# Kernel optimization log

Hardware: AMD Instinct MI355X
Metric: run time of the kernel (lower is better)

The kernel has to match this reference:

```python
import jax, jax.numpy as jnp
import numpy as np

N = 1_000_000      # total action rows
S = 250_000        # number of segments (intersections)
D_IN = 64
D_H = 128


def _res_block(x, W, b, P=None):
    # y = relu(x @ W + b); residual add (projected if dims differ)
    y = jax.nn.relu(x @ W + b)
    res = x if P is None else x @ P
    return y + res


def setup_inputs() -> dict:
    key = jax.random.key(0)
    ks = jax.random.split(key, 16)
    sc = 0.02
    x = jax.random.normal(ks[0], (N, D_IN), dtype=jnp.float32)
    index = jnp.sort(jax.random.randint(ks[1], (N,), 0, S)).astype(jnp.int64)
    return {
        "x": x,
        "index": index,
        # value in-stack (1 block, D_IN -> D_H, projected residual)
        "v_in_W": jax.random.normal(ks[2], (D_IN, D_H), jnp.float32) * sc,
        "v_in_b": jnp.zeros((D_H,), jnp.float32),
        "v_in_P": jax.random.normal(ks[3], (D_IN, D_H), jnp.float32) * sc,
        # value out-stack (1 block, D_H -> D_H, identity residual)
        "v_out_W": jax.random.normal(ks[4], (D_H, D_H), jnp.float32) * sc,
        "v_out_b": jnp.zeros((D_H,), jnp.float32),
        # value head linear D_H -> 1
        "v_lin_W": jax.random.normal(ks[5], (D_H, 1), jnp.float32) * sc,
        "v_lin_b": jnp.zeros((1,), jnp.float32),
        # advantage stack (2 blocks: D_IN->D_H projected, D_H->D_H identity)
        "a_W0": jax.random.normal(ks[6], (D_IN, D_H), jnp.float32) * sc,
        "a_b0": jnp.zeros((D_H,), jnp.float32),
        "a_P0": jax.random.normal(ks[7], (D_IN, D_H), jnp.float32) * sc,
        "a_W1": jax.random.normal(ks[8], (D_H, D_H), jnp.float32) * sc,
        "a_b1": jnp.zeros((D_H,), jnp.float32),
        # advantage head linear D_H -> 1
        "a_lin_W": jax.random.normal(ks[9], (D_H, 1), jnp.float32) * sc,
        "a_lin_b": jnp.zeros((1,), jnp.float32),
    }


def reference(x, index, v_in_W, v_in_b, v_in_P, v_out_W, v_out_b, v_lin_W,
              v_lin_b, a_W0, a_b0, a_P0, a_W1, a_b1, a_lin_W, a_lin_b):
    idx = index.astype(jnp.int32)

    # ---- value stream ----
    h = _res_block(x, v_in_W, v_in_b, v_in_P)               # [N, D_H]
    agg = jax.ops.segment_sum(h, idx, num_segments=S)       # [S, D_H]
    h2 = _res_block(agg, v_out_W, v_out_b)                  # [S, D_H]
    sv = h2 @ v_lin_W + v_lin_b                             # [S, 1]
    state_values = sv[idx]                                  # [N, 1] gather-back

    # ---- advantage stream ----
    a = _res_block(x, a_W0, a_b0, a_P0)                     # [N, D_H]
    a = _res_block(a, a_W1, a_b1)                           # [N, D_H]
    adv = a @ a_lin_W + a_lin_b                             # [N, 1]
    ones = jnp.ones((adv.shape[0],), adv.dtype)
    cnt = jax.ops.segment_sum(ones, idx, num_segments=S)    # [S]
    seg_sum = jax.ops.segment_sum(adv, idx, num_segments=S)  # [S, 1]
    seg_mean = seg_sum / jnp.maximum(cnt, 1.0)[:, None]      # [S, 1]
    adv_centered = adv - seg_mean[idx]                       # [N, 1]

    action_values = (state_values + adv_centered).squeeze(-1)  # [N]
    return action_values, index
```

## Files before the change

kernel.cpp:

```cpp
#include <hip/hip_runtime.h>

typedef _Float16 f16;
typedef _Float16 f16x8 __attribute__((ext_vector_type(8)));
typedef _Float16 f16x4v __attribute__((ext_vector_type(4)));
typedef float    f32x4 __attribute__((ext_vector_type(4)));
typedef int      i32x4 __attribute__((ext_vector_type(4)));

#define NROWS 1000000
#define DIN   64
#define DH    128
#define SEGS  250000
#define SPB   64

#define MFMA16(a, b, c) __builtin_amdgcn_mfma_f32_16x16x32_f16((a), (b), (c), 0, 0, 0)

__global__ void k_bounds(const int* __restrict__ idx,
                         int* __restrict__ row_start, int N) {
  int r = blockIdx.x * blockDim.x + threadIdx.x;
  if (r >= N) return;
  int cur  = min(max(idx[r], 0), SEGS - 1);
  int prev = (r == 0) ? -1 : min(max(idx[r - 1], 0), SEGS - 1);
  for (int s = prev + 1; s <= cur; ++s) row_start[s] = r;
  if (r == N - 1) {
    for (int s = cur + 1; s <= SEGS; ++s) row_start[s] = N;
  }
}

__global__ void k_pack(const float* __restrict__ W, f16* __restrict__ out, int K) {
  const int T = K >> 5;
  int i = blockIdx.x * blockDim.x + threadIdx.x;
  if (i >= K * DH) return;
  int e = i & 7, l = (i >> 3) & 63, f = i >> 9;
  int t = f % T, cb = f / T;
  int k = t * 32 + ((l >> 4) << 3) + e;
  int c = cb * 16 + (l & 15);
  out[i] = (f16)W[k * DH + c];
}

__device__ __forceinline__ f16x8 ldfrag(const f16* __restrict__ p, int f, int lane) {
  return *(const f16x8*)(p + (((size_t)f * 64 + lane) << 3));
}

__device__ __forceinline__ f16x8 cvt8(f32x4 u0, f32x4 u1) {
  f16x8 r;
  r[0] = (f16)u0[0]; r[1] = (f16)u0[1]; r[2] = (f16)u0[2]; r[3] = (f16)u0[3];
  r[4] = (f16)u1[0]; r[5] = (f16)u1[1]; r[6] = (f16)u1[2]; r[7] = (f16)u1[3];
  return r;
}

__global__ __launch_bounds__(512) void k_fused(
    const float* __restrict__ x, const int* __restrict__ idx,
    const int* __restrict__ row_start,
    const f16* __restrict__ vWp, const f16* __restrict__ vPp,
    const f16* __restrict__ aW0p, const f16* __restrict__ aP0p,
    const f16* __restrict__ aW1p, const f16* __restrict__ voWp,
    const float* __restrict__ vb,  const float* __restrict__ vob,
    const float* __restrict__ vlW, const float* __restrict__ vlb,
    const float* __restrict__ ab0, const float* __restrict__ ab1,
    const float* __restrict__ alW, const float* __restrict__ alb,
    float* __restrict__ out)
{
  __shared__ __align__(16) f16   xb16[2][4096];
  __shared__ __align__(16) f16   Ash[16 * 512];
  __shared__ __align__(16) f16   Hsh[16 * 512];
  __shared__ __align__(16) f16   IndSh[8 * 512];
  __shared__ __align__(16) int   segsh[2][64];
  __shared__ __align__(16) float advp[8][64];
  __shared__ float advsum_sh[SPB];
  __shared__ float corr_sh[SPB];

  const int tid  = threadIdx.x;
  const int wave = tid >> 6, lane = tid & 63;
  const int lg = lane >> 4, lm = lane & 15;
  const int s0 = blockIdx.x * SPB;
  const int send = min(s0 + SPB, SEGS);
  const int rbeg = row_start[s0], rend = row_start[send];

  const int srow_t = tid >> 3;
  const int sc8    = tid & 7;
  const int swz    = ((sc8 ^ (srow_t & 7)) * 16) + srow_t * 128;

  const int btgt = (wave & 3) * 16 + lm;
  const int bsrc = (wave >> 2) * 32 + lg * 8;

  float b0r[4], b1r[4], alwr[4];
#pragma unroll
  for (int q = 0; q < 4; ++q) {
    const int ch = wave * 16 + lg * 4 + q;
    b0r[q] = ab0[ch]; b1r[q] = ab1[ch]; alwr[q] = alW[ch];
  }
  const int ccol = wave * 16 + lm;
  const float vbr  = vb[ccol];
  const float vobr = vob[ccol];
  const float vlwr = vlW[ccol];
  const float alb0 = alb[0], vlb0 = vlb[0];

  f16x8 bW[2], bP[2], w0t[2], p0t[2];
#pragma unroll
  for (int t = 0; t < 2; ++t) {
    bW [t] = ldfrag(vWp,  wave * 2 + t, lane);
    bP [t] = ldfrag(vPp,  wave * 2 + t, lane);
    w0t[t] = ldfrag(aW0p, wave * 2 + t, lane);
    p0t[t] = ldfrag(aP0p, wave * 2 + t, lane);
  }

  f32x4 agg_c[4];
#pragma unroll
  for (int rf = 0; rf < 4; ++rf) { f32x4 z = {0.f,0.f,0.f,0.f}; agg_c[rf] = z; }

  if (tid < SPB) advsum_sh[tid] = 0.f;

  if (rbeg < rend) {
    const float* src = x + (size_t)min(rbeg + srow_t, NROWS - 1) * DIN + sc8 * 8;
    f32x4 u0 = *(const f32x4*)(src);
    f32x4 u1 = *(const f32x4*)(src + 4);
    *(f16x8*)((char*)&xb16[0][0] + swz) = cvt8(u0, u1);
  }
  if (tid < 64) {
    const int n0 = min(64, rend - rbeg);
    int sr = idx[min(rbeg + tid, NROWS - 1)];
    segsh[0][tid] = (tid < n0 && n0 > 0) ? sr - s0 : -1;
  }
  __syncthreads();

  int par = 0;
  for (int rt = rbeg; rt < rend; rt += 64, par ^= 1) {
    const int nrows = min(64, rend - rt);
    const bool has_next = (rt + 64) < rend;
    const int nrows_next = has_next ? min(64, rend - rt - 64) : 0;

    const int seg_raw = idx[min(rt + 64 + tid, NROWS - 1)];

    f32x4 xr0, xr1;
    if (has_next) {
      const float* src = x + (size_t)min(rt + 64 + srow_t, NROWS - 1) * DIN + sc8 * 8;
      xr0 = *(const f32x4*)(src);
      xr1 = *(const f32x4*)(src + 4);
    }

    {
      const i32x4 sa = *(const i32x4*)&segsh[par][bsrc];
      const i32x4 sb = *(const i32x4*)&segsh[par][bsrc + 4];
      f16x8 iv;
#pragma unroll
      for (int e = 0; e < 4; ++e) {
        iv[e]     = (sa[e] == btgt) ? (f16)1.f : (f16)0.f;
        iv[e + 4] = (sb[e] == btgt) ? (f16)1.f : (f16)0.f;
      }
      *(f16x8*)&IndSh[(wave * 64 + lane) * 8] = iv;
    }

    f16x8 ax[4][2];
#pragma unroll
    for (int rf = 0; rf < 4; ++rf) {
      const int row = rf * 16 + lm;
      const int rbase = row * 128;
      const int rsw = row & 7;
#pragma unroll
      for (int t = 0; t < 2; ++t)
        ax[rf][t] = *(const f16x8*)((const char*)&xb16[par][0] +
                                    rbase + ((t * 4 + lg) ^ rsw) * 16);
    }

    f16x8 hb[2];
    {
      f32x4 cA[4], cB[4];
#pragma unroll
      for (int rf = 0; rf < 4; ++rf) { f32x4 z = {0.f,0.f,0.f,0.f}; cA[rf] = z; cB[rf] = z; }
#pragma unroll
      for (int t = 0; t < 2; ++t)
#pragma unroll
        for (int rf = 0; rf < 4; ++rf) {
          cA[rf] = MFMA16(ax[rf][t], bW[t], cA[rf]);
          cB[rf] = MFMA16(ax[rf][t], bP[t], cB[rf]);
        }
#pragma unroll
      for (int rf = 0; rf < 4; ++rf) {
        f16x4v hv;
#pragma unroll
        for (int q = 0; q < 4; ++q)
          hv[q] = (f16)(fmaxf(cA[rf][q] + vbr, 0.f) + cB[rf][q]);
        const int laneb = ((rf & 1) * 2 + (lg >> 1)) * 16 + lm;
        const int off = ((wave * 2 + (rf >> 1)) * 64 + laneb) * 8 + (lg & 1) * 4;
        *(f16x4v*)&Hsh[off] = hv;
      }
#pragma unroll
      for (int t = 0; t < 2; ++t)
        hb[t] = *(const f16x8*)&Hsh[((wave * 2 + t) * 64 + lane) * 8];
    }

    float pA[4] = {0.f, 0.f, 0.f, 0.f};
    {
      f32x4 cA2[4], cB2[4];
#pragma unroll
      for (int cfr = 0; cfr < 4; ++cfr) { f32x4 z = {0.f,0.f,0.f,0.f}; cA2[cfr] = z; cB2[cfr] = z; }
#pragma unroll
      for (int t = 0; t < 2; ++t)
#pragma unroll
        for (int cfr = 0; cfr < 4; ++cfr) {
          cA2[cfr] = MFMA16(w0t[t], ax[cfr][t], cA2[cfr]);
          cB2[cfr] = MFMA16(p0t[t], ax[cfr][t], cB2[cfr]);
        }
#pragma unroll
      for (int cfr = 0; cfr < 4; ++cfr) {
        f16x4v av;
#pragma unroll
        for (int q = 0; q < 4; ++q) {
          float a1 = fmaxf(cA2[cfr][q] + b0r[q], 0.f) + cB2[cfr][q];
          pA[cfr] += a1 * alwr[q];
          av[q] = (f16)a1;
        }
        const int lane_a = lm + 16 * ((wave & 1) * 2 + (lg >> 1));
        const int off = ((cfr * 4 + (wave >> 1)) * 64 + lane_a) * 8 + (lg & 1) * 4;
        *(f16x4v*)&Ash[off] = av;
      }
    }

    f16x8 w1[4];
#pragma unroll
    for (int t = 0; t < 4; ++t)
      w1[t] = ldfrag(aW1p, wave * 4 + t, lane);

    asm volatile("s_waitcnt lgkmcnt(0)" ::: "memory");
    __builtin_amdgcn_s_barrier();

#pragma unroll
    for (int t = 0; t < 2; ++t)
#pragma unroll
      for (int rf = 0; rf < 4; ++rf) {
        const f16x8 ind = *(const f16x8*)&IndSh[((t * 4 + rf) * 64 + lane) * 8];
        agg_c[rf] = MFMA16(ind, hb[t], agg_c[rf]);
      }

    {
      f32x4 c2[4];
#pragma unroll
      for (int cfr = 0; cfr < 4; ++cfr) { f32x4 z = {0.f,0.f,0.f,0.f}; c2[cfr] = z; }
#pragma unroll
      for (int t = 0; t < 4; ++t)
#pragma unroll
        for (int cfr = 0; cfr < 4; ++cfr) {
          const f16x8 bv = *(const f16x8*)&Ash[((cfr * 4 + t) * 64 + lane) * 8];
          c2[cfr] = MFMA16(w1[t], bv, c2[cfr]);
        }
#pragma unroll
      for (int cfr = 0; cfr < 4; ++cfr) {
        float s = pA[cfr];
#pragma unroll
        for (int q = 0; q < 4; ++q)
          s += fmaxf(c2[cfr][q] + b1r[q], 0.f) * alwr[q];
        s += __shfl_xor(s, 16);
        s += __shfl_xor(s, 32);
        if (lg == 0) advp[wave][cfr * 16 + lm] = s;
      }
    }

    if (has_next)
      *(f16x8*)((char*)&xb16[par ^ 1][0] + swz) = cvt8(xr0, xr1);
    if (tid < 64) segsh[par ^ 1][tid] = (tid < nrows_next) ? seg_raw - s0 : -1;

    __syncthreads();

    if (wave == 2) {
      const int r = lane;
      const bool valid = r < nrows;
      const int sg = valid ? segsh[par][r] : -1;
      float acc = 0.f;
      if (valid) {
        float adv = advp[0][r] + advp[1][r] + advp[2][r] + advp[3][r] +
                    advp[4][r] + advp[5][r] + advp[6][r] + advp[7][r] + alb0;
        out[rt + r] = adv;
        acc = adv;
      }
#pragma unroll
      for (int d = 1; d < 64; d <<= 1) {
        float nv = __shfl_down(acc, d);
        int   ns = __shfl_down(sg, d);
        if (r + d < 64 && ns == sg) acc += nv;
      }
      if (valid && (r == 0 || segsh[par][r - 1] != sg)) advsum_sh[sg] += acc;
    }
  }

  __syncthreads();
#pragma unroll
  for (int rf = 0; rf < 4; ++rf) {
#pragma unroll
    for (int q = 0; q < 4; ++q)
      Ash[((rf * 4 + (wave >> 1)) * 64 +
           ((wave & 1) * 2 + (lm >> 3)) * 16 + (lg * 4 + q)) * 8 + (lm & 7)] =
        (f16)agg_c[rf][q];
  }
  __syncthreads();

  {
    f16x8 bvo[4];
#pragma unroll
    for (int t = 0; t < 4; ++t)
      bvo[t] = ldfrag(voWp, wave * 4 + t, lane);
    f32x4 c3[4];
#pragma unroll
    for (int rf = 0; rf < 4; ++rf) { f32x4 z = {0.f,0.f,0.f,0.f}; c3[rf] = z; }
#pragma unroll
    for (int rf = 0; rf < 4; ++rf)
#pragma unroll
      for (int t = 0; t < 4; ++t) {
        const f16x8 av = *(const f16x8*)&Ash[((rf * 4 + t) * 64 + lane) * 8];
        c3[rf] = MFMA16(av, bvo[t], c3[rf]);
      }
    f32x4 p3[4];
#pragma unroll
    for (int rf = 0; rf < 4; ++rf)
#pragma unroll
      for (int q = 0; q < 4; ++q) {
        float h2 = fmaxf(c3[rf][q] + vobr, 0.f) + agg_c[rf][q];
        p3[rf][q] = h2 * vlwr;
      }
#pragma unroll
    for (int m = 1; m <= 8; m <<= 1)
#pragma unroll
      for (int rf = 0; rf < 4; ++rf)
#pragma unroll
        for (int q = 0; q < 4; ++q)
          p3[rf][q] += __shfl_xor(p3[rf][q], m);
    if (lm == 0) {
#pragma unroll
      for (int rf = 0; rf < 4; ++rf)
        *(f32x4*)&advp[wave][rf * 16 + lg * 4] = p3[rf];
    }
  }
  __syncthreads();

  if (tid < send - s0) {
    float sv = advp[0][tid] + advp[1][tid] + advp[2][tid] + advp[3][tid] +
               advp[4][tid] + advp[5][tid] + advp[6][tid] + advp[7][tid] + vlb0;
    int cnt = row_start[s0 + tid + 1] - row_start[s0 + tid];
    corr_sh[tid] = sv - advsum_sh[tid] / (float)max(cnt, 1);
  }
  __syncthreads();

  for (int r = rbeg + tid; r < rend; r += 512) {
    const int s = idx[r];
    out[r] += corr_sh[s - s0];
    out[NROWS + r] = (float)s;
  }
}

extern "C" void kernel_launch(void* const* d_in, const int* in_sizes, int n_in,
                              void* d_out, int out_size, void* d_ws, size_t ws_size,
                              hipStream_t stream) {
  (void)n_in; (void)out_size; (void)ws_size;
  const float* x   = (const float*)d_in[0];
  const int*   idx = (const int*)d_in[1];
  const float* vW  = (const float*)d_in[2];
  const float* vb  = (const float*)d_in[3];
  const float* vP  = (const float*)d_in[4];
  const float* voW = (const float*)d_in[5];
  const float* vob = (const float*)d_in[6];
  const float* vlW = (const float*)d_in[7];
  const float* vlb = (const float*)d_in[8];
  const float* aW0 = (const float*)d_in[9];
  const float* ab0 = (const float*)d_in[10];
  const float* aP0 = (const float*)d_in[11];
  const float* aW1 = (const float*)d_in[12];
  const float* ab1 = (const float*)d_in[13];
  const float* alW = (const float*)d_in[14];
  const float* alb = (const float*)d_in[15];

  const int N = in_sizes[0] / DIN;
  float* out = (float*)d_out;

  int* row_start = (int*)d_ws;
  char* pkbase = (char*)d_ws + (((SEGS + 1) * 4 + 127) & ~127);
  f16* vWp  = (f16*)pkbase;
  f16* vPp  = vWp  + 8192;
  f16* aW0p = vPp  + 8192;
  f16* aP0p = aW0p + 8192;
  f16* aW1p = aP0p + 8192;
  f16* voWp = aW1p + 16384;

  k_bounds<<<(N + 255) / 256, 256, 0, stream>>>(idx, row_start, N);
  k_pack<<<32, 256, 0, stream>>>(vW,  vWp,  64);
  k_pack<<<32, 256, 0, stream>>>(vP,  vPp,  64);
  k_pack<<<32, 256, 0, stream>>>(aW0, aW0p, 64);
  k_pack<<<32, 256, 0, stream>>>(aP0, aP0p, 64);
  k_pack<<<64, 256, 0, stream>>>(aW1, aW1p, 128);
  k_pack<<<64, 256, 0, stream>>>(voW, voWp, 128);

  const int nblk = (SEGS + SPB - 1) / SPB;
  k_fused<<<nblk, 512, 0, stream>>>(x, idx, row_start,
                                    vWp, vPp, aW0p, aP0p, aW1p, voWp,
                                    vb, vob, vlW, vlb, ab0, ab1, alW, alb,
                                    out);
}
```

Measured before the change: 264.6 us.

## Double-buffer LDS scratch to drop one barrier per row tile

```diff
diff --git a/kernel.cpp b/kernel.cpp
--- a/kernel.cpp
+++ b/kernel.cpp
@@ -61,11 +61,11 @@
     float* __restrict__ out)
 {
   __shared__ __align__(16) f16   xb16[2][4096];
-  __shared__ __align__(16) f16   Ash[16 * 512];
-  __shared__ __align__(16) f16   Hsh[16 * 512];
-  __shared__ __align__(16) f16   IndSh[8 * 512];
-  __shared__ __align__(16) int   segsh[2][64];
-  __shared__ __align__(16) float advp[8][64];
+  __shared__ __align__(16) f16   Ash[2][8192];
+  __shared__ __align__(16) f16   Hsh[8192];
+  __shared__ __align__(16) f16   IndSh[2][4096];
+  __shared__ __align__(16) int   segsh[4][64];
+  __shared__ __align__(16) float advp[2][8][64];
   __shared__ float advsum_sh[SPB];
   __shared__ float corr_sh[SPB];
 
@@ -121,33 +121,38 @@
     int sr = idx[min(rbeg + tid, NROWS - 1)];
     segsh[0][tid] = (tid < n0 && n0 > 0) ? sr - s0 : -1;
   }
+  f32x4 xr0, xr1;
+  int seg_raw;
+  {
+    const float* src = x + (size_t)min(rbeg + 64 + srow_t, NROWS - 1) * DIN + sc8 * 8;
+    xr0 = *(const f32x4*)(src);
+    xr1 = *(const f32x4*)(src + 4);
+    seg_raw = idx[min(rbeg + 64 + tid, NROWS - 1)];
+  }
   __syncthreads();
 
-  int par = 0;
-  for (int rt = rbeg; rt < rend; rt += 64, par ^= 1) {
+  int t = 0, fin_rt = rbeg, fin_nrows = 0;
+  for (int rt = rbeg; rt < rend; rt += 64, ++t) {
     const int nrows = min(64, rend - rt);
     const bool has_next = (rt + 64) < rend;
     const int nrows_next = has_next ? min(64, rend - rt - 64) : 0;
-
-    const int seg_raw = idx[min(rt + 64 + tid, NROWS - 1)];
-
-    f32x4 xr0, xr1;
-    if (has_next) {
-      const float* src = x + (size_t)min(rt + 64 + srow_t, NROWS - 1) * DIN + sc8 * 8;
-      xr0 = *(const f32x4*)(src);
-      xr1 = *(const f32x4*)(src + 4);
-    }
+    const int sc_ = t & 1;
+
+    if (has_next)
+      *(f16x8*)((char*)&xb16[sc_ ^ 1][0] + swz) = cvt8(xr0, xr1);
+    if (tid < 64)
+      segsh[(t + 1) & 3][tid] = (tid < nrows_next) ? seg_raw - s0 : -1;
 
     {
-      const i32x4 sa = *(const i32x4*)&segsh[par][bsrc];
-      const i32x4 sb = *(const i32x4*)&segsh[par][bsrc + 4];
+      const i32x4 sa = *(const i32x4*)&segsh[t & 3][bsrc];
+      const i32x4 sb = *(const i32x4*)&segsh[t & 3][bsrc + 4];
       f16x8 iv;
 #pragma unroll
       for (int e = 0; e < 4; ++e) {
         iv[e]     = (sa[e] == btgt) ? (f16)1.f : (f16)0.f;
         iv[e + 4] = (sb[e] == btgt) ? (f16)1.f : (f16)0.f;
       }
-      *(f16x8*)&IndSh[(wave * 64 + lane) * 8] = iv;
+      *(f16x8*)&IndSh[sc_][(wave * 64 + lane) * 8] = iv;
     }
 
     f16x8 ax[4][2];
@@ -157,9 +162,9 @@
       const int rbase = row * 128;
       const int rsw = row & 7;
 #pragma unroll
-      for (int t = 0; t < 2; ++t)
-        ax[rf][t] = *(const f16x8*)((const char*)&xb16[par][0] +
-                                    rbase + ((t * 4 + lg) ^ rsw) * 16);
+      for (int tt = 0; tt < 2; ++tt)
+        ax[rf][tt] = *(const f16x8*)((const char*)&xb16[sc_][0] +
+                                     rbase + ((tt * 4 + lg) ^ rsw) * 16);
     }
 
     f16x8 hb[2];
@@ -168,11 +173,11 @@
 #pragma unroll
       for (int rf = 0; rf < 4; ++rf) { f32x4 z = {0.f,0.f,0.f,0.f}; cA[rf] = z; cB[rf] = z; }
 #pragma unroll
-      for (int t = 0; t < 2; ++t)
+      for (int tt = 0; tt < 2; ++tt)
 #pragma unroll
         for (int rf = 0; rf < 4; ++rf) {
-          cA[rf] = MFMA16(ax[rf][t], bW[t], cA[rf]);
-          cB[rf] = MFMA16(ax[rf][t], bP[t], cB[rf]);
+          cA[rf] = MFMA16(ax[rf][tt], bW[tt], cA[rf]);
+          cB[rf] = MFMA16(ax[rf][tt], bP[tt], cB[rf]);
         }
 #pragma unroll
       for (int rf = 0; rf < 4; ++rf) {
@@ -185,8 +190,8 @@
         *(f16x4v*)&Hsh[off] = hv;
       }
 #pragma unroll
-      for (int t = 0; t < 2; ++t)
-        hb[t] = *(const f16x8*)&Hsh[((wave * 2 + t) * 64 + lane) * 8];
+      for (int tt = 0; tt < 2; ++tt)
+        hb[tt] = *(const f16x8*)&Hsh[((wave * 2 + tt) * 64 + lane) * 8];
     }
 
     float pA[4] = {0.f, 0.f, 0.f, 0.f};
@@ -195,11 +200,11 @@
 #pragma unroll
       for (int cfr = 0; cfr < 4; ++cfr) { f32x4 z = {0.f,0.f,0.f,0.f}; cA2[cfr] = z; cB2[cfr] = z; }
 #pragma unroll
-      for (int t = 0; t < 2; ++t)
+      for (int tt = 0; tt < 2; ++tt)
 #pragma unroll
         for (int cfr = 0; cfr < 4; ++cfr) {
-          cA2[cfr] = MFMA16(w0t[t], ax[cfr][t], cA2[cfr]);
-          cB2[cfr] = MFMA16(p0t[t], ax[cfr][t], cB2[cfr]);
+          cA2[cfr] = MFMA16(w0t[tt], ax[cfr][tt], cA2[cfr]);
+          cB2[cfr] = MFMA16(p0t[tt], ax[cfr][tt], cB2[cfr]);
         }
 #pragma unroll
       for (int cfr = 0; cfr < 4; ++cfr) {
@@ -212,24 +217,46 @@
         }
         const int lane_a = lm + 16 * ((wave & 1) * 2 + (lg >> 1));
         const int off = ((cfr * 4 + (wave >> 1)) * 64 + lane_a) * 8 + (lg & 1) * 4;
-        *(f16x4v*)&Ash[off] = av;
+        *(f16x4v*)&Ash[sc_][off] = av;
       }
     }
 
     f16x8 w1[4];
 #pragma unroll
-    for (int t = 0; t < 4; ++t)
-      w1[t] = ldfrag(aW1p, wave * 4 + t, lane);
+    for (int tt = 0; tt < 4; ++tt)
+      w1[tt] = ldfrag(aW1p, wave * 4 + tt, lane);
 
     asm volatile("s_waitcnt lgkmcnt(0)" ::: "memory");
     __builtin_amdgcn_s_barrier();
 
-#pragma unroll
-    for (int t = 0; t < 2; ++t)
+    if (wave == 2 && t > 0) {
+      const int r = lane;
+      const bool valid = r < fin_nrows;
+      const int sg = valid ? segsh[(t - 1) & 3][r] : -1;
+      float acc = 0.f;
+      if (valid) {
+        float adv = advp[sc_ ^ 1][0][r] + advp[sc_ ^ 1][1][r] +
+                    advp[sc_ ^ 1][2][r] + advp[sc_ ^ 1][3][r] +
+                    advp[sc_ ^ 1][4][r] + advp[sc_ ^ 1][5][r] +
+                    advp[sc_ ^ 1][6][r] + advp[sc_ ^ 1][7][r] + alb0;
+        out[fin_rt + r] = adv;
+        acc = adv;
+      }
+#pragma unroll
+      for (int d = 1; d < 64; d <<= 1) {
+        float nv = __shfl_down(acc, d);
+        int   ns = __shfl_down(sg, d);
+        if (r + d < 64 && ns == sg) acc += nv;
+      }
+      if (valid && (r == 0 || segsh[(t - 1) & 3][r - 1] != sg)) advsum_sh[sg] += acc;
+    }
+
+#pragma unroll
+    for (int tt = 0; tt < 2; ++tt)
 #pragma unroll
       for (int rf = 0; rf < 4; ++rf) {
-        const f16x8 ind = *(const f16x8*)&IndSh[((t * 4 + rf) * 64 + lane) * 8];
-        agg_c[rf] = MFMA16(ind, hb[t], agg_c[rf]);
+        const f16x8 ind = *(const f16x8*)&IndSh[sc_][((tt * 4 + rf) * 64 + lane) * 8];
+        agg_c[rf] = MFMA16(ind, hb[tt], agg_c[rf]);
       }
 
     {
@@ -237,11 +264,11 @@
 #pragma unroll
       for (int cfr = 0; cfr < 4; ++cfr) { f32x4 z = {0.f,0.f,0.f,0.f}; c2[cfr] = z; }
 #pragma unroll
-      for (int t = 0; t < 4; ++t)
+      for (int tt = 0; tt < 4; ++tt)
 #pragma unroll
         for (int cfr = 0; cfr < 4; ++cfr) {
-          const f16x8 bv = *(const f16x8*)&Ash[((cfr * 4 + t) * 64 + lane) * 8];
-          c2[cfr] = MFMA16(w1[t], bv, c2[cfr]);
+          const f16x8 bv = *(const f16x8*)&Ash[sc_][((cfr * 4 + tt) * 64 + lane) * 8];
+          c2[cfr] = MFMA16(w1[tt], bv, c2[cfr]);
         }
 #pragma unroll
       for (int cfr = 0; cfr < 4; ++cfr) {
@@ -251,44 +278,50 @@
           s += fmaxf(c2[cfr][q] + b1r[q], 0.f) * alwr[q];
         s += __shfl_xor(s, 16);
         s += __shfl_xor(s, 32);
-        if (lg == 0) advp[wave][cfr * 16 + lm] = s;
-      }
-    }
-
-    if (has_next)
-      *(f16x8*)((char*)&xb16[par ^ 1][0] + swz) = cvt8(xr0, xr1);
-    if (tid < 64) segsh[par ^ 1][tid] = (tid < nrows_next) ? seg_raw - s0 : -1;
-
-    __syncthreads();
-
-    if (wave == 2) {
-      const int r = lane;
-      const bool valid = r < nrows;
-      const int sg = valid ? segsh[par][r] : -1;
-      float acc = 0.f;
-      if (valid) {
-        float adv = advp[0][r] + advp[1][r] + advp[2][r] + advp[3][r] +
-                    advp[4][r] + advp[5][r] + advp[6][r] + advp[7][r] + alb0;
-        out[rt + r] = adv;
-        acc = adv;
-      }
-#pragma unroll
-      for (int d = 1; d < 64; d <<= 1) {
-        float nv = __shfl_down(acc, d);
-        int   ns = __shfl_down(sg, d);
-        if (r + d < 64 && ns == sg) acc += nv;
-      }
-      if (valid && (r == 0 || segsh[par][r - 1] != sg)) advsum_sh[sg] += acc;
-    }
+        if (lg == 0) advp[sc_][wave][cfr * 16 + lm] = s;
+      }
+    }
+
+    if (rt + 128 < rend) {
+      const float* src = x + (size_t)min(rt + 128 + srow_t, NROWS - 1) * DIN + sc8 * 8;
+      xr0 = *(const f32x4*)(src);
+      xr1 = *(const f32x4*)(src + 4);
+    }
+    seg_raw = idx[min(rt + 128 + tid, NROWS - 1)];
+
+    fin_rt = rt; fin_nrows = nrows;
   }
 
   __syncthreads();
+  if (wave == 2 && t > 0) {
+    const int tl = t - 1;
+    const int r = lane;
+    const bool valid = r < fin_nrows;
+    const int sg = valid ? segsh[tl & 3][r] : -1;
+    float acc = 0.f;
+    if (valid) {
+      float adv = advp[tl & 1][0][r] + advp[tl & 1][1][r] +
+                  advp[tl & 1][2][r] + advp[tl & 1][3][r] +
+                  advp[tl & 1][4][r] + advp[tl & 1][5][r] +
+                  advp[tl & 1][6][r] + advp[tl & 1][7][r] + alb0;
+      out[fin_rt + r] = adv;
+      acc = adv;
+    }
+#pragma unroll
+    for (int d = 1; d < 64; d <<= 1) {
+      float nv = __shfl_down(acc, d);
+      int   ns = __shfl_down(sg, d);
+      if (r + d < 64 && ns == sg) acc += nv;
+    }
+    if (valid && (r == 0 || segsh[tl & 3][r - 1] != sg)) advsum_sh[sg] += acc;
+  }
+
 #pragma unroll
   for (int rf = 0; rf < 4; ++rf) {
 #pragma unroll
     for (int q = 0; q < 4; ++q)
-      Ash[((rf * 4 + (wave >> 1)) * 64 +
-           ((wave & 1) * 2 + (lm >> 3)) * 16 + (lg * 4 + q)) * 8 + (lm & 7)] =
+      Ash[0][((rf * 4 + (wave >> 1)) * 64 +
+              ((wave & 1) * 2 + (lm >> 3)) * 16 + (lg * 4 + q)) * 8 + (lm & 7)] =
         (f16)agg_c[rf][q];
   }
   __syncthreads();
@@ -296,17 +329,17 @@
   {
     f16x8 bvo[4];
 #pragma unroll
-    for (int t = 0; t < 4; ++t)
-      bvo[t] = ldfrag(voWp, wave * 4 + t, lane);
+    for (int tt = 0; tt < 4; ++tt)
+      bvo[tt] = ldfrag(voWp, wave * 4 + tt, lane);
     f32x4 c3[4];
 #pragma unroll
     for (int rf = 0; rf < 4; ++rf) { f32x4 z = {0.f,0.f,0.f,0.f}; c3[rf] = z; }
 #pragma unroll
     for (int rf = 0; rf < 4; ++rf)
 #pragma unroll
-      for (int t = 0; t < 4; ++t) {
-        const f16x8 av = *(const f16x8*)&Ash[((rf * 4 + t) * 64 + lane) * 8];
-        c3[rf] = MFMA16(av, bvo[t], c3[rf]);
+      for (int tt = 0; tt < 4; ++tt) {
+        const f16x8 av = *(const f16x8*)&Ash[0][((rf * 4 + tt) * 64 + lane) * 8];
+        c3[rf] = MFMA16(av, bvo[tt], c3[rf]);
       }
     f32x4 p3[4];
 #pragma unroll
@@ -326,14 +359,14 @@
     if (lm == 0) {
 #pragma unroll
       for (int rf = 0; rf < 4; ++rf)
-        *(f32x4*)&advp[wave][rf * 16 + lg * 4] = p3[rf];
+        *(f32x4*)&advp[0][wave][rf * 16 + lg * 4] = p3[rf];
     }
   }
   __syncthreads();
 
   if (tid < send - s0) {
-    float sv = advp[0][tid] + advp[1][tid] + advp[2][tid] + advp[3][tid] +
-               advp[4][tid] + advp[5][tid] + advp[6][tid] + advp[7][tid] + vlb0;
+    float sv = advp[0][0][tid] + advp[0][1][tid] + advp[0][2][tid] + advp[0][3][tid] +
+               advp[0][4][tid] + advp[0][5][tid] + advp[0][6][tid] + advp[0][7][tid] + vlb0;
     int cnt = row_start[s0 + tid + 1] - row_start[s0 + tid];
     corr_sh[tid] = sv - advsum_sh[tid] / (float)max(cnt, 1);
   }
```

Result: slower. 276.4 us (+4.5%).

## Process 128 rows per loop iteration as two 64-row sub-tiles

Applied to the files above, without the earlier changes.

```diff
diff --git a/kernel.cpp b/kernel.cpp
--- a/kernel.cpp
+++ b/kernel.cpp
@@ -60,12 +60,12 @@
     const float* __restrict__ alW, const float* __restrict__ alb,
     float* __restrict__ out)
 {
-  __shared__ __align__(16) f16   xb16[2][4096];
-  __shared__ __align__(16) f16   Ash[16 * 512];
+  __shared__ __align__(16) f16   xb16[2][8192];
+  __shared__ __align__(16) f16   Ash[2][8192];
   __shared__ __align__(16) f16   Hsh[16 * 512];
-  __shared__ __align__(16) f16   IndSh[8 * 512];
-  __shared__ __align__(16) int   segsh[2][64];
-  __shared__ __align__(16) float advp[8][64];
+  __shared__ __align__(16) f16   IndSh[2][4096];
+  __shared__ __align__(16) int   segsh[2][128];
+  __shared__ __align__(16) float advp[2][8][64];
   __shared__ float advsum_sh[SPB];
   __shared__ float corr_sh[SPB];
 
@@ -76,9 +76,10 @@
   const int send = min(s0 + SPB, SEGS);
   const int rbeg = row_start[s0], rend = row_start[send];
 
-  const int srow_t = tid >> 3;
-  const int sc8    = tid & 7;
-  const int swz    = ((sc8 ^ (srow_t & 7)) * 16) + srow_t * 128;
+  const int srow_t = tid >> 2;
+  const int scp    = (tid & 3) * 2;
+  const int swz0   = ((scp ^ (srow_t & 7)) * 16) + srow_t * 128;
+  const int swz1   = (((scp + 1) ^ (srow_t & 7)) * 16) + srow_t * 128;
 
   const int btgt = (wave & 3) * 16 + lm;
   const int bsrc = (wave >> 2) * 32 + lg * 8;
@@ -111,108 +112,119 @@
   if (tid < SPB) advsum_sh[tid] = 0.f;
 
   if (rbeg < rend) {
-    const float* src = x + (size_t)min(rbeg + srow_t, NROWS - 1) * DIN + sc8 * 8;
+    const float* src = x + (size_t)min(rbeg + srow_t, NROWS - 1) * DIN + (tid & 3) * 16;
     f32x4 u0 = *(const f32x4*)(src);
     f32x4 u1 = *(const f32x4*)(src + 4);
-    *(f16x8*)((char*)&xb16[0][0] + swz) = cvt8(u0, u1);
-  }
-  if (tid < 64) {
-    const int n0 = min(64, rend - rbeg);
+    f32x4 u2 = *(const f32x4*)(src + 8);
+    f32x4 u3 = *(const f32x4*)(src + 12);
+    *(f16x8*)((char*)&xb16[0][0] + swz0) = cvt8(u0, u1);
+    *(f16x8*)((char*)&xb16[0][0] + swz1) = cvt8(u2, u3);
+  }
+  if (tid < 128) {
+    const int n0 = min(128, rend - rbeg);
     int sr = idx[min(rbeg + tid, NROWS - 1)];
     segsh[0][tid] = (tid < n0 && n0 > 0) ? sr - s0 : -1;
   }
   __syncthreads();
 
   int par = 0;
-  for (int rt = rbeg; rt < rend; rt += 64, par ^= 1) {
-    const int nrows = min(64, rend - rt);
-    const bool has_next = (rt + 64) < rend;
-    const int nrows_next = has_next ? min(64, rend - rt - 64) : 0;
-
-    const int seg_raw = idx[min(rt + 64 + tid, NROWS - 1)];
-
-    f32x4 xr0, xr1;
+  for (int rt = rbeg; rt < rend; rt += 128, par ^= 1) {
+    const int nrows = min(128, rend - rt);
+    const bool has_next = (rt + 128) < rend;
+    const int nrows_next = has_next ? min(128, rend - rt - 128) : 0;
+
+    const int seg_raw = idx[min(rt + 128 + tid, NROWS - 1)];
+
+    f32x4 xr0, xr1, xr2, xr3;
     if (has_next) {
-      const float* src = x + (size_t)min(rt + 64 + srow_t, NROWS - 1) * DIN + sc8 * 8;
+      const float* src = x + (size_t)min(rt + 128 + srow_t, NROWS - 1) * DIN + (tid & 3) * 16;
       xr0 = *(const f32x4*)(src);
       xr1 = *(const f32x4*)(src + 4);
-    }
-
-    {
-      const i32x4 sa = *(const i32x4*)&segsh[par][bsrc];
-      const i32x4 sb = *(const i32x4*)&segsh[par][bsrc + 4];
+      xr2 = *(const f32x4*)(src + 8);
+      xr3 = *(const f32x4*)(src + 12);
+    }
+
+#pragma unroll
+    for (int sub = 0; sub < 2; ++sub) {
+      const i32x4 sa = *(const i32x4*)&segsh[par][sub * 64 + bsrc];
+      const i32x4 sb = *(const i32x4*)&segsh[par][sub * 64 + bsrc + 4];
       f16x8 iv;
 #pragma unroll
       for (int e = 0; e < 4; ++e) {
         iv[e]     = (sa[e] == btgt) ? (f16)1.f : (f16)0.f;
         iv[e + 4] = (sb[e] == btgt) ? (f16)1.f : (f16)0.f;
       }
-      *(f16x8*)&IndSh[(wave * 64 + lane) * 8] = iv;
-    }
-
-    f16x8 ax[4][2];
-#pragma unroll
-    for (int rf = 0; rf < 4; ++rf) {
-      const int row = rf * 16 + lm;
-      const int rbase = row * 128;
-      const int rsw = row & 7;
-#pragma unroll
-      for (int t = 0; t < 2; ++t)
-        ax[rf][t] = *(const f16x8*)((const char*)&xb16[par][0] +
-                                    rbase + ((t * 4 + lg) ^ rsw) * 16);
-    }
-
-    f16x8 hb[2];
-    {
-      f32x4 cA[4], cB[4];
-#pragma unroll
-      for (int rf = 0; rf < 4; ++rf) { f32x4 z = {0.f,0.f,0.f,0.f}; cA[rf] = z; cB[rf] = z; }
-#pragma unroll
-      for (int t = 0; t < 2; ++t)
+      *(f16x8*)&IndSh[sub][(wave * 64 + lane) * 8] = iv;
+    }
+
+    f16x8 hb[2][2];
+    float pA[2][4];
+#pragma unroll
+    for (int sub = 0; sub < 2; ++sub) {
+      f16x8 ax[4][2];
+#pragma unroll
+      for (int rf = 0; rf < 4; ++rf) {
+        const int row = sub * 64 + rf * 16 + lm;
+        const int rbase = row * 128;
+        const int rsw = row & 7;
+#pragma unroll
+        for (int t = 0; t < 2; ++t)
+          ax[rf][t] = *(const f16x8*)((const char*)&xb16[par][0] +
+                                      rbase + ((t * 4 + lg) ^ rsw) * 16);
+      }
+
+      {
+        f32x4 cA[4], cB[4];
+#pragma unroll
+        for (int rf = 0; rf < 4; ++rf) { f32x4 z = {0.f,0.f,0.f,0.f}; cA[rf] = z; cB[rf] = z; }
+#pragma unroll
+        for (int t = 0; t < 2; ++t)
+#pragma unroll
+          for (int rf = 0; rf < 4; ++rf) {
+            cA[rf] = MFMA16(ax[rf][t], bW[t], cA[rf]);
+            cB[rf] = MFMA16(ax[rf][t], bP[t], cB[rf]);
+          }
 #pragma unroll
         for (int rf = 0; rf < 4; ++rf) {
-          cA[rf] = MFMA16(ax[rf][t], bW[t], cA[rf]);
-          cB[rf] = MFMA16(ax[rf][t], bP[t], cB[rf]);
+          f16x4v hv;
+#pragma unroll
+          for (int q = 0; q < 4; ++q)
+            hv[q] = (f16)(fmaxf(cA[rf][q] + vbr, 0.f) + cB[rf][q]);
+          const int laneb = ((rf & 1) * 2 + (lg >> 1)) * 16 + lm;
+          const int off = ((wave * 2 + (rf >> 1)) * 64 + laneb) * 8 + (lg & 1) * 4;
+          *(f16x4v*)&Hsh[off] = hv;
         }
 #pragma unroll
-      for (int rf = 0; rf < 4; ++rf) {
-        f16x4v hv;
-#pragma unroll
-        for (int q = 0; q < 4; ++q)
-          hv[q] = (f16)(fmaxf(cA[rf][q] + vbr, 0.f) + cB[rf][q]);
-        const int laneb = ((rf & 1) * 2 + (lg >> 1)) * 16 + lm;
-        const int off = ((wave * 2 + (rf >> 1)) * 64 + laneb) * 8 + (lg & 1) * 4;
-        *(f16x4v*)&Hsh[off] = hv;
-      }
-#pragma unroll
-      for (int t = 0; t < 2; ++t)
-        hb[t] = *(const f16x8*)&Hsh[((wave * 2 + t) * 64 + lane) * 8];
-    }
-
-    float pA[4] = {0.f, 0.f, 0.f, 0.f};
-    {
-      f32x4 cA2[4], cB2[4];
-#pragma unroll
-      for (int cfr = 0; cfr < 4; ++cfr) { f32x4 z = {0.f,0.f,0.f,0.f}; cA2[cfr] = z; cB2[cfr] = z; }
-#pragma unroll
-      for (int t = 0; t < 2; ++t)
+        for (int t = 0; t < 2; ++t)
+          hb[sub][t] = *(const f16x8*)&Hsh[((wave * 2 + t) * 64 + lane) * 8];
+      }
+
+      {
+        f32x4 cA2[4], cB2[4];
+#pragma unroll
+        for (int cfr = 0; cfr < 4; ++cfr) { f32x4 z = {0.f,0.f,0.f,0.f}; cA2[cfr] = z; cB2[cfr] = z; }
+#pragma unroll
+        for (int t = 0; t < 2; ++t)
+#pragma unroll
+          for (int cfr = 0; cfr < 4; ++cfr) {
+            cA2[cfr] = MFMA16(w0t[t], ax[cfr][t], cA2[cfr]);
+            cB2[cfr] = MFMA16(p0t[t], ax[cfr][t], cB2[cfr]);
+          }
 #pragma unroll
         for (int cfr = 0; cfr < 4; ++cfr) {
-          cA2[cfr] = MFMA16(w0t[t], ax[cfr][t], cA2[cfr]);
-          cB2[cfr] = MFMA16(p0t[t], ax[cfr][t], cB2[cfr]);
+          f16x4v av;
+          float s = 0.f;
+#pragma unroll
+          for (int q = 0; q < 4; ++q) {
+            float a1 = fmaxf(cA2[cfr][q] + b0r[q], 0.f) + cB2[cfr][q];
+            s += a1 * alwr[q];
+            av[q] = (f16)a1;
+          }
+          pA[sub][cfr] = s;
+          const int lane_a = lm + 16 * ((wave & 1) * 2 + (lg >> 1));
+          const int off = ((cfr * 4 + (wave >> 1)) * 64 + lane_a) * 8 + (lg & 1) * 4;
+          *(f16x4v*)&Ash[sub][off] = av;
         }
-#pragma unroll
-      for (int cfr = 0; cfr < 4; ++cfr) {
-        f16x4v av;
-#pragma unroll
-        for (int q = 0; q < 4; ++q) {
-          float a1 = fmaxf(cA2[cfr][q] + b0r[q], 0.f) + cB2[cfr][q];
-          pA[cfr] += a1 * alwr[q];
-          av[q] = (f16)a1;
-        }
-        const int lane_a = lm + 16 * ((wave & 1) * 2 + (lg >> 1));
-        const int off = ((cfr * 4 + (wave >> 1)) * 64 + lane_a) * 8 + (lg & 1) * 4;
-        *(f16x4v*)&Ash[off] = av;
       }
     }
 
@@ -225,14 +237,17 @@
     __builtin_amdgcn_s_barrier();
 
 #pragma unroll
-    for (int t = 0; t < 2; ++t)
-#pragma unroll
-      for (int rf = 0; rf < 4; ++rf) {
-        const f16x8 ind = *(const f16x8*)&IndSh[((t * 4 + rf) * 64 + lane) * 8];
-        agg_c[rf] = MFMA16(ind, hb[t], agg_c[rf]);
-      }
-
-    {
+    for (int sub = 0; sub < 2; ++sub)
+#pragma unroll
+      for (int t = 0; t < 2; ++t)
+#pragma unroll
+        for (int rf = 0; rf < 4; ++rf) {
+          const f16x8 ind = *(const f16x8*)&IndSh[sub][((t * 4 + rf) * 64 + lane) * 8];
+          agg_c[rf] = MFMA16(ind, hb[sub][t], agg_c[rf]);
+        }
+
+#pragma unroll
+    for (int sub = 0; sub < 2; ++sub) {
       f32x4 c2[4];
 #pragma unroll
       for (int cfr = 0; cfr < 4; ++cfr) { f32x4 z = {0.f,0.f,0.f,0.f}; c2[cfr] = z; }
@@ -240,36 +255,41 @@
       for (int t = 0; t < 4; ++t)
 #pragma unroll
         for (int cfr = 0; cfr < 4; ++cfr) {
-          const f16x8 bv = *(const f16x8*)&Ash[((cfr * 4 + t) * 64 + lane) * 8];
+          const f16x8 bv = *(const f16x8*)&Ash[sub][((cfr * 4 + t) * 64 + lane) * 8];
           c2[cfr] = MFMA16(w1[t], bv, c2[cfr]);
         }
 #pragma unroll
       for (int cfr = 0; cfr < 4; ++cfr) {
-        float s = pA[cfr];
+        float s = pA[sub][cfr];
 #pragma unroll
         for (int q = 0; q < 4; ++q)
           s += fmaxf(c2[cfr][q] + b1r[q], 0.f) * alwr[q];
         s += __shfl_xor(s, 16);
         s += __shfl_xor(s, 32);
-        if (lg == 0) advp[wave][cfr * 16 + lm] = s;
-      }
-    }
-
-    if (has_next)
-      *(f16x8*)((char*)&xb16[par ^ 1][0] + swz) = cvt8(xr0, xr1);
-    if (tid < 64) segsh[par ^ 1][tid] = (tid < nrows_next) ? seg_raw - s0 : -1;
+        if (lg == 0) advp[sub][wave][cfr * 16 + lm] = s;
+      }
+    }
+
+    if (has_next) {
+      *(f16x8*)((char*)&xb16[par ^ 1][0] + swz0) = cvt8(xr0, xr1);
+      *(f16x8*)((char*)&xb16[par ^ 1][0] + swz1) = cvt8(xr2, xr3);
+    }
+    if (tid < 128) segsh[par ^ 1][tid] = (tid < nrows_next) ? seg_raw - s0 : -1;
 
     __syncthreads();
 
-    if (wave == 2) {
+    if (wave == 2 || wave == 3) {
+      const int sub = wave - 2;
+      const int base = sub * 64;
       const int r = lane;
-      const bool valid = r < nrows;
-      const int sg = valid ? segsh[par][r] : -1;
+      const int nrs = min(64, max(0, nrows - base));
+      const bool valid = r < nrs;
+      const int sg = valid ? segsh[par][base + r] : -1;
       float acc = 0.f;
       if (valid) {
-        float adv = advp[0][r] + advp[1][r] + advp[2][r] + advp[3][r] +
-                    advp[4][r] + advp[5][r] + advp[6][r] + advp[7][r] + alb0;
-        out[rt + r] = adv;
+        float adv = advp[sub][0][r] + advp[sub][1][r] + advp[sub][2][r] + advp[sub][3][r] +
+                    advp[sub][4][r] + advp[sub][5][r] + advp[sub][6][r] + advp[sub][7][r] + alb0;
+        out[rt + base + r] = adv;
         acc = adv;
       }
 #pragma unroll
@@ -278,7 +298,8 @@
         int   ns = __shfl_down(sg, d);
         if (r + d < 64 && ns == sg) acc += nv;
       }
-      if (valid && (r == 0 || segsh[par][r - 1] != sg)) advsum_sh[sg] += acc;
+      if (valid && (r == 0 || segsh[par][base + r - 1] != sg))
+        atomicAdd(&advsum_sh[sg], acc);
     }
   }
 
@@ -287,8 +308,8 @@
   for (int rf = 0; rf < 4; ++rf) {
 #pragma unroll
     for (int q = 0; q < 4; ++q)
-      Ash[((rf * 4 + (wave >> 1)) * 64 +
-           ((wave & 1) * 2 + (lm >> 3)) * 16 + (lg * 4 + q)) * 8 + (lm & 7)] =
+      Ash[0][((rf * 4 + (wave >> 1)) * 64 +
+              ((wave & 1) * 2 + (lm >> 3)) * 16 + (lg * 4 + q)) * 8 + (lm & 7)] =
         (f16)agg_c[rf][q];
   }
   __syncthreads();
@@ -305,7 +326,7 @@
     for (int rf = 0; rf < 4; ++rf)
 #pragma unroll
       for (int t = 0; t < 4; ++t) {
-        const f16x8 av = *(const f16x8*)&Ash[((rf * 4 + t) * 64 + lane) * 8];
+        const f16x8 av = *(const f16x8*)&Ash[0][((rf * 4 + t) * 64 + lane) * 8];
         c3[rf] = MFMA16(av, bvo[t], c3[rf]);
       }
     f32x4 p3[4];
@@ -326,14 +347,14 @@
     if (lm == 0) {
 #pragma unroll
       for (int rf = 0; rf < 4; ++rf)
-        *(f32x4*)&advp[wave][rf * 16 + lg * 4] = p3[rf];
+        *(f32x4*)&advp[0][wave][rf * 16 + lg * 4] = p3[rf];
     }
   }
   __syncthreads();
 
   if (tid < send - s0) {
-    float sv = advp[0][tid] + advp[1][tid] + advp[2][tid] + advp[3][tid] +
-               advp[4][tid] + advp[5][tid] + advp[6][tid] + advp[7][tid] + vlb0;
+    float sv = advp[0][0][tid] + advp[0][1][tid] + advp[0][2][tid] + advp[0][3][tid] +
+               advp[0][4][tid] + advp[0][5][tid] + advp[0][6][tid] + advp[0][7][tid] + vlb0;
     int cnt = row_start[s0 + tid + 1] - row_start[s0 + tid];
     corr_sh[tid] = sv - advsum_sh[tid] / (float)max(cnt, 1);
   }
```

New measurement: 287.4 us. +8.6%, slower.
